# Performance work log

Hardware: AMD Instinct MI355X
Metric: run time of the kernel (lower is better)

Reference implementation:

```python
import jax, jax.numpy as jnp
import numpy as np

NUM_HEADS = 16
HEAD_DIM = 64


def setup_inputs() -> dict:
    key = jax.random.key(0)
    k1, k2, k3 = jax.random.split(key, 3)
    B, S, D = 2, 2048, 1024
    scale = 1.0 / np.sqrt(D)
    return {
        "x": jax.random.normal(k1, (B, S, D), dtype=jnp.float32),
        "W_qkv": jax.random.normal(k2, (D, 3 * D), dtype=jnp.float32) * scale,
        "b_qkv": jnp.zeros((3 * D,), dtype=jnp.float32),
        "W_o": jax.random.normal(k3, (D, D), dtype=jnp.float32) * scale,
        "b_o": jnp.zeros((D,), dtype=jnp.float32),
    }


def reference(x, W_qkv, b_qkv, W_o, b_o):
    B, S, D = x.shape
    H, Hd = NUM_HEADS, HEAD_DIM
    qkv = x @ W_qkv + b_qkv                      # [B, S, 3D]
    qkv = qkv.reshape(B, S, H, 3 * Hd).transpose(0, 2, 1, 3)  # [B, H, S, 3Hd]
    q, k, v = jnp.split(qkv, 3, axis=-1)         # each [B, H, S, Hd]
    # negative squared Euclidean distance: -(|q|^2 - 2 q.k + |k|^2)
    q_sq = jnp.sum(q * q, axis=-1)[..., :, None]   # [B, H, S, 1]
    k_sq = jnp.sum(k * k, axis=-1)[..., None, :]   # [B, H, 1, S]
    qk = jnp.einsum("bhsd,bhtd->bhst", q, k)       # [B, H, S, S]
    logits = -(q_sq - 2.0 * qk + k_sq)
    attn = jax.nn.softmax(logits, axis=-1)
    vals = jnp.einsum("bhst,bhtd->bhsd", attn, v)  # [B, H, S, Hd]
    vals = vals.transpose(0, 2, 1, 3).reshape(B, S, D)
    return vals @ W_o + b_o
```

## Files before the change

kernel.cpp:

```cpp
#include <hip/hip_runtime.h>
#include <hip/hip_bf16.h>

#define NUM_B   2
#define SEQ     2048
#define DMODEL  1024
#define NH      16
#define HD      64
#define M_TOT   (NUM_B * SEQ)
#define N_QKV   (3 * DMODEL)
#define LOG2E   1.4426950408889634f
#define EXP_BIAS 96.0f

typedef __attribute__((ext_vector_type(8))) short short8v;
typedef __attribute__((ext_vector_type(4))) float float4v;
typedef unsigned short ushort_t;

__device__ __forceinline__ ushort_t f2bf(float x) {
    unsigned u = __builtin_bit_cast(unsigned, x);
    u = u + 0x7FFFu + ((u >> 16) & 1u);
    return (ushort_t)(u >> 16);
}
__device__ __forceinline__ float bf2f(ushort_t h) {
    unsigned u = ((unsigned)h) << 16;
    return __builtin_bit_cast(float, u);
}
__device__ __forceinline__ void gll16(const void* g, void* l) {
    __builtin_amdgcn_global_load_lds(
        (const __attribute__((address_space(1))) unsigned int*)g,
        (__attribute__((address_space(3))) unsigned int*)l, 16, 0, 0);
}
__device__ __forceinline__ int sw4(int r) { return (r & 3) ^ ((r >> 2) & 3); }

__global__ __launch_bounds__(256) void prep_kernel(
    const float* __restrict__ Wq, const float* __restrict__ Wo,
    const float* __restrict__ Xf,
    ushort_t* __restrict__ WqT_hi, ushort_t* __restrict__ WqT_lo,
    ushort_t* __restrict__ WoT,
    ushort_t* __restrict__ Xhi, ushort_t* __restrict__ Xlo)
{
    const int bid = blockIdx.x;
    const int t = threadIdx.x;

    if (bid >= 1024) {
        size_t base = (size_t)(bid - 1024) * 4096 + t * 16;
        float xs[16];
        *(float4v*)&xs[0]  = *(const float4v*)(Xf + base);
        *(float4v*)&xs[4]  = *(const float4v*)(Xf + base + 4);
        *(float4v*)&xs[8]  = *(const float4v*)(Xf + base + 8);
        *(float4v*)&xs[12] = *(const float4v*)(Xf + base + 12);
        short8v h0, h1, l0, l1;
        #pragma unroll
        for (int e = 0; e < 8; e++) {
            ushort_t a = f2bf(xs[e]), b = f2bf(xs[8 + e]);
            h0[e] = (short)a; h1[e] = (short)b;
            l0[e] = (short)f2bf(xs[e] - bf2f(a));
            l1[e] = (short)f2bf(xs[8 + e] - bf2f(b));
        }
        *(short8v*)(Xhi + base) = h0; *(short8v*)(Xhi + base + 8) = h1;
        *(short8v*)(Xlo + base) = l0; *(short8v*)(Xlo + base + 8) = l1;
        return;
    }

    __shared__ float Tf[64][65];
    const float* src; ushort_t *dhi, *dlo; int N, k0, n0;
    if (bid < 768) {
        int kt = bid / 48, nt = bid % 48;
        src = Wq; N = N_QKV; dhi = WqT_hi; dlo = WqT_lo;
        k0 = kt * 64; n0 = nt * 64;
    } else {
        int tid = bid - 768;
        int kt = tid >> 4, nt = tid & 15;
        src = Wo; N = DMODEL; dhi = WoT; dlo = nullptr;
        k0 = kt * 64; n0 = nt * 64;
    }
    {
        int r = t >> 2, c0 = (t & 3) * 16;
        const float* srow = src + (size_t)(k0 + r) * N + n0 + c0;
        #pragma unroll
        for (int u = 0; u < 4; u++) {
            float4v f = *(const float4v*)(srow + 4 * u);
            #pragma unroll
            for (int e = 0; e < 4; e++) Tf[r][c0 + 4 * u + e] = f[e];
        }
    }
    __syncthreads();
    {
        int nl = t >> 2, kc = (t & 3) * 16;
        short8v h0, h1, l0, l1;
        #pragma unroll
        for (int e = 0; e < 8; e++) {
            float x0 = Tf[kc + e][nl];
            float x1 = Tf[kc + 8 + e][nl];
            ushort_t a = f2bf(x0), b = f2bf(x1);
            h0[e] = (short)a; h1[e] = (short)b;
            l0[e] = (short)f2bf(x0 - bf2f(a));
            l1[e] = (short)f2bf(x1 - bf2f(b));
        }
        ushort_t* o = dhi + (size_t)(n0 + nl) * 1024 + k0 + kc;
        *(short8v*)o = h0; *(short8v*)(o + 8) = h1;
        if (dlo) {
            ushort_t* o2 = dlo + (size_t)(n0 + nl) * 1024 + k0 + kc;
            *(short8v*)o2 = l0; *(short8v*)(o2 + 8) = l1;
        }
    }
}

__global__ __launch_bounds__(512, 2) void qkv_mfma256_kernel(
    const ushort_t* __restrict__ Xhi, const ushort_t* __restrict__ Xlo,
    const ushort_t* __restrict__ WqT_hi, const ushort_t* __restrict__ WqT_lo,
    const float* __restrict__ bias,
    ushort_t* __restrict__ Qhi, ushort_t* __restrict__ Qlo,
    ushort_t* __restrict__ Khi, ushort_t* __restrict__ Klo,
    ushort_t* __restrict__ Vout,
    float* __restrict__ Qsq, float* __restrict__ Ksq)
{
    __shared__ ushort_t AS [2 * 2 * 8192];
    __shared__ ushort_t BSh[2 * 2 * 8192];
    const int SLAB = 8192;
    const int BUFS = 2 * SLAB;

    const int t    = threadIdx.x;
    const int w    = t >> 6;
    const int quad = (t >> 4) & 3, ln = t & 15;
    const int wr = w >> 2, wc = w & 3;
    const int bx = blockIdx.x, by = blockIdx.y;
    const int p  = bx >> 2, bq = bx & 3;
    const int m0 = by * 256;
    const bool qk = (p != 2);
    const int h  = 4 * bq + wc;
    const int g  = p + 3 * h;

    const ushort_t* gA[2]; const ushort_t* gB[2]; int lOff[2];
    #pragma unroll
    for (int i = 0; i < 2; i++) {
        int c = 512 * i + t;
        int r = c >> 2, kb = c & 3;
        gA[i] = Xhi + (size_t)(m0 + r) * 1024 + 8 * (kb ^ sw4(r));
        int hj = 4 * bq + (r >> 6);
        int ng = 192 * hj + 64 * p + (r & 63);
        gB[i] = WqT_hi + (size_t)ng * 1024 + 8 * (kb ^ sw4(r));
        lOff[i] = (512 * i + 64 * w) * 8;
    }
    const size_t xlo_off = (size_t)(Xlo - Xhi);
    const size_t wlo_off = (size_t)(WqT_lo - WqT_hi);

    int aoff[8], boff[4];
    #pragma unroll
    for (int mt = 0; mt < 8; mt++) {
        int m_l = 128 * wr + 16 * mt + ln;
        aoff[mt] = m_l * 32 + ((quad ^ sw4(m_l)) << 3);
    }
    #pragma unroll
    for (int nt = 0; nt < 4; nt++) {
        int n_l = 64 * wc + 16 * nt + ln;
        boff[nt] = n_l * 32 + ((quad ^ sw4(n_l)) << 3);
    }

    float4v acc[8][4];
    #pragma unroll
    for (int i = 0; i < 8; i++)
        #pragma unroll
        for (int j = 0; j < 4; j++) acc[i][j] = (float4v){0.f, 0.f, 0.f, 0.f};

    auto stage = [&](int ks, int buf) {
        const int kk = 32 * ks;
        ushort_t* Ab = &AS [buf * BUFS];
        ushort_t* Bb = &BSh[buf * BUFS];
        #pragma unroll
        for (int i = 0; i < 2; i++) {
            gll16(gA[i] + kk, Ab + lOff[i]);
            gll16(gB[i] + kk, Bb + lOff[i]);
        }
        if (qk) {
            #pragma unroll
            for (int i = 0; i < 2; i++) {
                gll16(gA[i] + kk + xlo_off, Ab + SLAB + lOff[i]);
                gll16(gB[i] + kk + wlo_off, Bb + SLAB + lOff[i]);
            }
        }
    };

    const int NKS = DMODEL / 32;
    stage(0, 0);
    __syncthreads();

    for (int ks = 0; ks < NKS; ks++) {
        const int buf = ks & 1;
        if (ks + 1 < NKS) stage(ks + 1, buf ^ 1);

        const ushort_t* Ab = &AS [buf * BUFS];
        const ushort_t* Bb = &BSh[buf * BUFS];

        short8v bh4[4], bl4[4];
        #pragma unroll
        for (int nt = 0; nt < 4; nt++) {
            bh4[nt] = *(const short8v*)(Bb + boff[nt]);
            if (qk) bl4[nt] = *(const short8v*)(Bb + SLAB + boff[nt]);
        }
        #pragma unroll
        for (int mt = 0; mt < 8; mt++) {
            short8v ahm = *(const short8v*)(Ab + aoff[mt]);
            if (qk) {
                short8v alm = *(const short8v*)(Ab + SLAB + aoff[mt]);
                #pragma unroll
                for (int nt = 0; nt < 4; nt++) {
                    acc[mt][nt] = __builtin_amdgcn_mfma_f32_16x16x32_bf16(ahm, bh4[nt], acc[mt][nt], 0, 0, 0);
                    acc[mt][nt] = __builtin_amdgcn_mfma_f32_16x16x32_bf16(ahm, bl4[nt], acc[mt][nt], 0, 0, 0);
                    acc[mt][nt] = __builtin_amdgcn_mfma_f32_16x16x32_bf16(alm, bh4[nt], acc[mt][nt], 0, 0, 0);
                }
            } else {
                #pragma unroll
                for (int nt = 0; nt < 4; nt++)
                    acc[mt][nt] = __builtin_amdgcn_mfma_f32_16x16x32_bf16(ahm, bh4[nt], acc[mt][nt], 0, 0, 0);
            }
        }
        __syncthreads();
    }

    float bvv[4];
    #pragma unroll
    for (int nt = 0; nt < 4; nt++) bvv[nt] = bias[64 * g + 16 * nt + ln];

    #pragma unroll
    for (int mt = 0; mt < 8; mt++) {
        #pragma unroll
        for (int r = 0; r < 4; r++) {
            int m = m0 + 128 * wr + 16 * mt + 4 * quad + r;
            int bb = m >> 11, s = m & (SEQ - 1);
            size_t hsrow = (size_t)(bb * NH + h) * SEQ + s;
            size_t rowbase = hsrow * HD;
            float vv[4];
            #pragma unroll
            for (int nt = 0; nt < 4; nt++) vv[nt] = acc[mt][nt][r] + bvv[nt];
            if (p == 0) {
                float sq = 0.f;
                #pragma unroll
                for (int nt = 0; nt < 4; nt++) {
                    float v = vv[nt];
                    sq += v * v;
                    float v2 = v * (2.0f * LOG2E);
                    ushort_t hb = f2bf(v2);
                    Qhi[rowbase + 16 * nt + ln] = hb;
                    Qlo[rowbase + 16 * nt + ln] = f2bf(v2 - bf2f(hb));
                }
                sq += __shfl_xor(sq, 1); sq += __shfl_xor(sq, 2);
                sq += __shfl_xor(sq, 4); sq += __shfl_xor(sq, 8);
                if (ln == 0) Qsq[hsrow] = sq * LOG2E - EXP_BIAS;
            } else if (p == 1) {
                float sq = 0.f;
                #pragma unroll
                for (int nt = 0; nt < 4; nt++) {
                    float v = vv[nt];
                    sq += v * v;
                    ushort_t hb = f2bf(v);
                    Khi[rowbase + 16 * nt + ln] = hb;
                    Klo[rowbase + 16 * nt + ln] = f2bf(v - bf2f(hb));
                }
                sq += __shfl_xor(sq, 1); sq += __shfl_xor(sq, 2);
                sq += __shfl_xor(sq, 4); sq += __shfl_xor(sq, 8);
                if (ln == 0) Ksq[hsrow] = sq * LOG2E;
            } else {
                #pragma unroll
                for (int nt = 0; nt < 4; nt++)
                    Vout[((size_t)(bb * NH + h) * 64 + 16 * nt + ln) * SEQ + s] = f2bf(vv[nt]);
            }
        }
    }
}

template<bool PRE>
__global__ __launch_bounds__(256) void qkv_mfma_kernel(
    const float* __restrict__ X,
    const ushort_t* __restrict__ Xhi, const ushort_t* __restrict__ Xlo,
    const ushort_t* __restrict__ WqT_hi, const ushort_t* __restrict__ WqT_lo,
    const float* __restrict__ bias,
    ushort_t* __restrict__ Qhi, ushort_t* __restrict__ Qlo,
    ushort_t* __restrict__ Khi, ushort_t* __restrict__ Klo,
    ushort_t* __restrict__ Vout,
    float* __restrict__ Qsq, float* __restrict__ Ksq)
{
    __shared__ ushort_t AS2[2 * 128 * 32];
    __shared__ ushort_t BS [2 * 128 * 32];
    const int LO = 128 * 32;
    const int t = threadIdx.x;
    const int w = t >> 6, lane = t & 63;
    const int quad = (t >> 4) & 3, ln = t & 15;
    const int wr = w >> 1, wc = w & 1;
    const int m0 = blockIdx.y * 128, n0 = blockIdx.x * 128;
    const int g = blockIdx.x * 2 + wc;
    const int h = g / 3, part = g % 3;

    const ushort_t* gA[2]; ushort_t* lA[2];
    const float* aptr = nullptr;
    ushort_t *ast_hi0, *ast_hi1, *ast_lo0, *ast_lo1;
    size_t xlo_off = 0;
    if constexpr (PRE) {
        #pragma unroll
        for (int i = 0; i < 2; i++) {
            int c = 256 * i + 64 * w + lane;
            int r = c >> 2, kbp = c & 3;
            gA[i] = Xhi + (size_t)(m0 + r) * 1024 + 8 * (kbp ^ sw4(r));
            lA[i] = &AS2[(256 * i + 64 * w) * 8];
        }
        xlo_off = (size_t)(Xlo - Xhi);
    } else {
        const int arow = t >> 1, akh = t & 1;
        aptr = X + (size_t)(m0 + arow) * DMODEL + 16 * akh;
        const int asw = sw4(arow);
        ast_hi0 = &AS2[arow * 32 + (((2 * akh) ^ asw) << 3)];
        ast_hi1 = &AS2[arow * 32 + (((2 * akh + 1) ^ asw) << 3)];
        ast_lo0 = &AS2[LO + arow * 32 + (((2 * akh) ^ asw) << 3)];
        ast_lo1 = &AS2[LO + arow * 32 + (((2 * akh + 1) ^ asw) << 3)];
    }

    const ushort_t* gB[2]; ushort_t* lB[2];
    #pragma unroll
    for (int i = 0; i < 2; i++) {
        int c = 256 * i + 64 * w + lane;
        int n = c >> 2, kbp = c & 3;
        gB[i] = WqT_hi + (size_t)(n0 + n) * 1024 + 8 * (kbp ^ sw4(n));
        lB[i] = &BS[(256 * i + 64 * w) * 8];
    }
    const size_t lo_goff = (size_t)(WqT_lo - WqT_hi);

    int aoff[4], boff[4];
    #pragma unroll
    for (int i = 0; i < 4; i++) {
        int m_l = 64 * wr + 16 * i + ln;
        aoff[i] = m_l * 32 + ((quad ^ sw4(m_l)) << 3);
        int n_l = 64 * wc + 16 * i + ln;
        boff[i] = n_l * 32 + ((quad ^ sw4(n_l)) << 3);
    }

    float4v acc[4][4];
    #pragma unroll
    for (int i = 0; i < 4; i++)
        #pragma unroll
        for (int j = 0; j < 4; j++) acc[i][j] = (float4v){0.f, 0.f, 0.f, 0.f};

    for (int k0 = 0; k0 < DMODEL; k0 += 32) {
        __syncthreads();
        #pragma unroll
        for (int i = 0; i < 2; i++) {
            gll16(gB[i] + k0, lB[i]);
            gll16(gB[i] + k0 + lo_goff, lB[i] + LO);
        }
        if constexpr (PRE) {
            #pragma unroll
            for (int i = 0; i < 2; i++) {
                gll16(gA[i] + k0, lA[i]);
                gll16(gA[i] + k0 + xlo_off, lA[i] + LO);
            }
        } else {
            float xs[16];
            *(float4v*)&xs[0]  = *(const float4v*)(aptr + k0);
            *(float4v*)&xs[4]  = *(const float4v*)(aptr + k0 + 4);
            *(float4v*)&xs[8]  = *(const float4v*)(aptr + k0 + 8);
            *(float4v*)&xs[12] = *(const float4v*)(aptr + k0 + 12);
            short8v h0, h1, l0, l1;
            #pragma unroll
            for (int e = 0; e < 8; e++) {
                ushort_t a = f2bf(xs[e]), b = f2bf(xs[8 + e]);
                h0[e] = (short)a; h1[e] = (short)b;
                l0[e] = (short)f2bf(xs[e] - bf2f(a));
                l1[e] = (short)f2bf(xs[8 + e] - bf2f(b));
            }
            *(short8v*)ast_hi0 = h0; *(short8v*)ast_hi1 = h1;
            *(short8v*)ast_lo0 = l0; *(short8v*)ast_lo1 = l1;
        }
        __syncthreads();

        short8v ah[4], al[4], bh[4], bl[4];
        #pragma unroll
        for (int i = 0; i < 4; i++) {
            ah[i] = *(short8v*)&AS2[aoff[i]];
            al[i] = *(short8v*)&AS2[LO + aoff[i]];
            bh[i] = *(short8v*)&BS[boff[i]];
            bl[i] = *(short8v*)&BS[LO + boff[i]];
        }
        if (part != 2) {
            #pragma unroll
            for (int mt = 0; mt < 4; mt++)
                #pragma unroll
                for (int nt = 0; nt < 4; nt++) {
                    acc[mt][nt] = __builtin_amdgcn_mfma_f32_16x16x32_bf16(ah[mt], bh[nt], acc[mt][nt], 0, 0, 0);
                    acc[mt][nt] = __builtin_amdgcn_mfma_f32_16x16x32_bf16(ah[mt], bl[nt], acc[mt][nt], 0, 0, 0);
                    acc[mt][nt] = __builtin_amdgcn_mfma_f32_16x16x32_bf16(al[mt], bh[nt], acc[mt][nt], 0, 0, 0);
                }
        } else {
            #pragma unroll
            for (int mt = 0; mt < 4; mt++)
                #pragma unroll
                for (int nt = 0; nt < 4; nt++)
                    acc[mt][nt] = __builtin_amdgcn_mfma_f32_16x16x32_bf16(ah[mt], bh[nt], acc[mt][nt], 0, 0, 0);
        }
    }

    float bvv[4];
    #pragma unroll
    for (int nt = 0; nt < 4; nt++) bvv[nt] = bias[64 * g + 16 * nt + ln];

    #pragma unroll
    for (int mt = 0; mt < 4; mt++) {
        #pragma unroll
        for (int r = 0; r < 4; r++) {
            int m = m0 + 64 * wr + 16 * mt + 4 * quad + r;
            int bb = m >> 11, s = m & (SEQ - 1);
            size_t hsrow = (size_t)(bb * NH + h) * SEQ + s;
            size_t rowbase = hsrow * HD;
            float vv[4];
            #pragma unroll
            for (int nt = 0; nt < 4; nt++) vv[nt] = acc[mt][nt][r] + bvv[nt];
            if (part == 0) {
                float sq = 0.f;
                #pragma unroll
                for (int nt = 0; nt < 4; nt++) {
                    float v = vv[nt];
                    sq += v * v;
                    float v2 = v * (2.0f * LOG2E);
                    ushort_t hb = f2bf(v2);
                    Qhi[rowbase + 16 * nt + ln] = hb;
                    Qlo[rowbase + 16 * nt + ln] = f2bf(v2 - bf2f(hb));
                }
                sq += __shfl_xor(sq, 1); sq += __shfl_xor(sq, 2);
                sq += __shfl_xor(sq, 4); sq += __shfl_xor(sq, 8);
                if (ln == 0) Qsq[hsrow] = sq * LOG2E - EXP_BIAS;
            } else if (part == 1) {
                float sq = 0.f;
                #pragma unroll
                for (int nt = 0; nt < 4; nt++) {
                    float v = vv[nt];
                    sq += v * v;
                    ushort_t hb = f2bf(v);
                    Khi[rowbase + 16 * nt + ln] = hb;
                    Klo[rowbase + 16 * nt + ln] = f2bf(v - bf2f(hb));
                }
                sq += __shfl_xor(sq, 1); sq += __shfl_xor(sq, 2);
                sq += __shfl_xor(sq, 4); sq += __shfl_xor(sq, 8);
                if (ln == 0) Ksq[hsrow] = sq * LOG2E;
            } else {
                #pragma unroll
                for (int nt = 0; nt < 4; nt++)
                    Vout[rowbase + 16 * nt + ln] = f2bf(vv[nt]);
            }
        }
    }
}

template<bool PRE>
__global__ __launch_bounds__(256, 4) void attn_mfma_kernel(
    const ushort_t* __restrict__ Qhi, const ushort_t* __restrict__ Qlo,
    const ushort_t* __restrict__ Khi, const ushort_t* __restrict__ Klo,
    const ushort_t* __restrict__ Vsrc,
    const float* __restrict__ Qsq, const float* __restrict__ Ksq,
    ushort_t* __restrict__ vals)
{
    __shared__ ushort_t KS[2 * 64 * 64];
    __shared__ ushort_t VtS [64 * 64];
    __shared__ ushort_t PsS [64 * 72];
    const int LO = 64 * 64;

    const int t    = threadIdx.x;
    const int w    = t >> 6, lane = t & 63;
    const int quad = (t >> 4) & 3, ln = t & 15;
    const int bh   = blockIdx.y;
    const int q0   = blockIdx.x * 64;
    const size_t base  = (size_t)bh * SEQ * HD;
    const size_t baseS = (size_t)bh * SEQ;

    short8v qhi[2], qlo[2];
    float4v qsq4;
    {
        size_t ro = base + (size_t)(q0 + 16 * w + ln) * HD + quad * 8;
        qhi[0] = *(const short8v*)(Qhi + ro);
        qhi[1] = *(const short8v*)(Qhi + ro + 32);
        qlo[0] = *(const short8v*)(Qlo + ro);
        qlo[1] = *(const short8v*)(Qlo + ro + 32);
        qsq4 = *(const float4v*)(Qsq + baseS + q0 + 16 * w + 4 * quad);
    }

    const ushort_t* gK[2]; ushort_t* lK[2];
    #pragma unroll
    for (int i = 0; i < 2; i++) {
        int c = 256 * i + 64 * w + lane;
        int key = c >> 3, dbp = c & 7;
        gK[i] = Khi + base + (size_t)key * HD + 8 * (dbp ^ (key & 7));
        lK[i] = &KS[(256 * i + 64 * w) * 8];
    }
    const size_t kloff = (size_t)(Klo - Khi);

    const ushort_t* gV[2]; ushort_t* lV[2];
    if constexpr (PRE) {
        #pragma unroll
        for (int i = 0; i < 2; i++) {
            int c = 256 * i + 64 * w + lane;
            int d = c >> 3, kc = c & 7;
            gV[i] = Vsrc + ((size_t)bh * 64 + d) * SEQ + 8 * (kc ^ (d & 7));
            lV[i] = &VtS[(256 * i + 64 * w) * 8];
        }
    }

    float4v accO[4];
    float lsum[4];
    #pragma unroll
    for (int nt = 0; nt < 4; nt++) accO[nt] = (float4v){0.f, 0.f, 0.f, 0.f};
    #pragma unroll
    for (int r = 0; r < 4; r++) lsum[r] = 0.f;

    for (int kt = 0; kt < SEQ; kt += 64) {
        __syncthreads();
        #pragma unroll
        for (int i = 0; i < 2; i++) {
            gll16(gK[i] + (size_t)kt * HD, lK[i]);
            gll16(gK[i] + (size_t)kt * HD + kloff, lK[i] + LO);
        }
        if constexpr (PRE) {
            #pragma unroll
            for (int i = 0; i < 2; i++)
                gll16(gV[i] + kt, lV[i]);
        } else {
            #pragma unroll
            for (int i = 0; i < 2; i++) {
                int c = t + 256 * i;
                int key = c >> 3, db = c & 7;
                short8v v8 = *(const short8v*)(Vsrc + base + (size_t)(kt + key) * HD + 8 * db);
                #pragma unroll
                for (int e = 0; e < 8; e++) {
                    int col = key ^ (e << 3);
                    VtS[(8 * db + e) * 64 + col] = (ushort_t)v8[e];
                }
            }
        }
        float ksq_c[4];
        #pragma unroll
        for (int nt = 0; nt < 4; nt++)
            ksq_c[nt] = Ksq[baseS + kt + 16 * nt + ln];
        __syncthreads();

        float4v accS[4];
        #pragma unroll
        for (int nt = 0; nt < 4; nt++) accS[nt] = (float4v){0.f, 0.f, 0.f, 0.f};

        #pragma unroll
        for (int nt = 0; nt < 4; nt++) {
            int keyrow = 16 * nt + ln;
            #pragma unroll
            for (int c = 0; c < 2; c++) {
                int db  = quad + 4 * c;
                int off = keyrow * 64 + ((db ^ (keyrow & 7)) << 3);
                short8v bh_ = *(short8v*)&KS[off];
                short8v bl_ = *(short8v*)&KS[LO + off];
                accS[nt] = __builtin_amdgcn_mfma_f32_16x16x32_bf16(qhi[c], bh_, accS[nt], 0, 0, 0);
                accS[nt] = __builtin_amdgcn_mfma_f32_16x16x32_bf16(qhi[c], bl_, accS[nt], 0, 0, 0);
                accS[nt] = __builtin_amdgcn_mfma_f32_16x16x32_bf16(qlo[c], bh_, accS[nt], 0, 0, 0);
            }
        }

        #pragma unroll
        for (int nt = 0; nt < 4; nt++) {
            float pv[4];
            #pragma unroll
            for (int r = 0; r < 4; r++) {
                float p = exp2f(accS[nt][r] - ksq_c[nt] - qsq4[r]);
                lsum[r] += p;
                pv[r] = p;
            }
            unsigned int pk01, pk23;
            asm("v_cvt_pk_bf16_f32 %0, %1, %2" : "=v"(pk01) : "v"(pv[0]), "v"(pv[1]));
            asm("v_cvt_pk_bf16_f32 %0, %1, %2" : "=v"(pk23) : "v"(pv[2]), "v"(pv[3]));
            ushort_t* pp = &PsS[(16 * w + 4 * quad) * 72 + 16 * nt + ln];
            pp[0]       = (ushort_t)(pk01 & 0xffffu);
            pp[72]      = (ushort_t)(pk01 >> 16);
            pp[144]     = (ushort_t)(pk23 & 0xffffu);
            pp[216]     = (ushort_t)(pk23 >> 16);
        }
        __syncthreads();

        #pragma unroll
        for (int c = 0; c < 2; c++) {
            short8v aP = *(short8v*)&PsS[(16 * w + ln) * 72 + quad * 8 + 32 * c];
            #pragma unroll
            for (int nt = 0; nt < 4; nt++) {
                int drow = 16 * nt + ln;
                int db   = quad + 4 * c;
                int off  = drow * 64 + ((db ^ (drow & 7)) << 3);
                short8v bV = *(short8v*)&VtS[off];
                accO[nt] = __builtin_amdgcn_mfma_f32_16x16x32_bf16(aP, bV, accO[nt], 0, 0, 0);
            }
        }
    }

    const int bb = bh >> 4, h = bh & 15;
    float inv[4];
    #pragma unroll
    for (int r = 0; r < 4; r++) {
        float s = lsum[r];
        s += __shfl_xor(s, 1); s += __shfl_xor(s, 2);
        s += __shfl_xor(s, 4); s += __shfl_xor(s, 8);
        inv[r] = 1.f / s;
    }
    #pragma unroll
    for (int nt = 0; nt < 4; nt++)
        #pragma unroll
        for (int r = 0; r < 4; r++) {
            int row = q0 + 16 * w + 4 * quad + r;
            vals[(size_t)(bb * SEQ + row) * DMODEL + h * 64 + 16 * nt + ln] =
                f2bf(accO[nt][r] * inv[r]);
        }
}

__global__ __launch_bounds__(256) void out_mfma_kernel(
    const ushort_t* __restrict__ Ab, const ushort_t* __restrict__ BT,
    const float* __restrict__ bias, float* __restrict__ out)
{
    __shared__ ushort_t AS[128 * 32], BSo[128 * 32];
    const int t = threadIdx.x;
    const int w = t >> 6, lane = t & 63;
    const int quad = (t >> 4) & 3, ln = t & 15;
    const int wr = w >> 1, wc = w & 1;
    const int m0 = blockIdx.y * 128, n0 = blockIdx.x * 128;

    const ushort_t* gA[2]; const ushort_t* gB[2];
    ushort_t *lA[2], *lB[2];
    #pragma unroll
    for (int i = 0; i < 2; i++) {
        int c = 256 * i + 64 * w + lane;
        int r = c >> 2, kbp = c & 3;
        gA[i] = Ab + (size_t)(m0 + r) * 1024 + 8 * (kbp ^ sw4(r));
        gB[i] = BT + (size_t)(n0 + r) * 1024 + 8 * (kbp ^ sw4(r));
        lA[i] = &AS[(256 * i + 64 * w) * 8];
        lB[i] = &BSo[(256 * i + 64 * w) * 8];
    }
    int aoff[4], boff[4];
    #pragma unroll
    for (int i = 0; i < 4; i++) {
        int m_l = 64 * wr + 16 * i + ln;
        aoff[i] = m_l * 32 + ((quad ^ sw4(m_l)) << 3);
        int n_l = 64 * wc + 16 * i + ln;
        boff[i] = n_l * 32 + ((quad ^ sw4(n_l)) << 3);
    }

    float4v acc[4][4];
    #pragma unroll
    for (int i = 0; i < 4; i++)
        #pragma unroll
        for (int j = 0; j < 4; j++) acc[i][j] = (float4v){0.f, 0.f, 0.f, 0.f};

    for (int k0 = 0; k0 < DMODEL; k0 += 32) {
        __syncthreads();
        #pragma unroll
        for (int i = 0; i < 2; i++) {
            gll16(gA[i] + k0, lA[i]);
            gll16(gB[i] + k0, lB[i]);
        }
        __syncthreads();
        short8v a[4], b[4];
        #pragma unroll
        for (int i = 0; i < 4; i++) {
            a[i] = *(short8v*)&AS[aoff[i]];
            b[i] = *(short8v*)&BSo[boff[i]];
        }
        #pragma unroll
        for (int mt = 0; mt < 4; mt++)
            #pragma unroll
            for (int nt = 0; nt < 4; nt++)
                acc[mt][nt] = __builtin_amdgcn_mfma_f32_16x16x32_bf16(a[mt], b[nt], acc[mt][nt], 0, 0, 0);
    }

    #pragma unroll
    for (int nt = 0; nt < 4; nt++) {
        int n = n0 + 64 * wc + 16 * nt + ln;
        float bv = bias[n];
        #pragma unroll
        for (int mt = 0; mt < 4; mt++)
            #pragma unroll
            for (int r = 0; r < 4; r++) {
                int m = m0 + 64 * wr + 16 * mt + 4 * quad + r;
                out[(size_t)m * DMODEL + n] = acc[mt][nt][r] + bv;
            }
    }
}

extern "C" void kernel_launch(void* const* d_in, const int* in_sizes, int n_in,
                              void* d_out, int out_size, void* d_ws, size_t ws_size,
                              hipStream_t stream) {
    const float* x     = (const float*)d_in[0];
    const float* W_qkv = (const float*)d_in[1];
    const float* b_qkv = (const float*)d_in[2];
    const float* W_o   = (const float*)d_in[3];
    const float* b_o   = (const float*)d_in[4];
    float* out = (float*)d_out;

    const size_t WQT = (size_t)N_QKV * DMODEL;
    const size_t WO  = (size_t)DMODEL * DMODEL;
    const size_t QE  = (size_t)NUM_B * NH * SEQ * HD;
    const size_t SQN = (size_t)NUM_B * NH * SEQ;

    const size_t NEED = (2 * WQT + WO + 5 * QE + 2 * QE) * 2 + 2 * SQN * 4;
    const bool pre = (ws_size >= NEED);

    ushort_t* ws     = (ushort_t*)d_ws;
    ushort_t* WqT_hi = ws;
    ushort_t* WqT_lo = WqT_hi + WQT;
    ushort_t* WoT    = WqT_lo + WQT;
    ushort_t* Qhi    = WoT + WO;
    ushort_t* Qlo    = Qhi + QE;
    ushort_t* Khi    = Qlo + QE;
    ushort_t* Klo    = Khi + QE;
    ushort_t* Vx     = Klo + QE;
    float*    Qsq; float* Ksq;
    ushort_t* valsb; ushort_t* Xhi = nullptr; ushort_t* Xlo = nullptr;

    if (pre) {
        Qsq   = (float*)(Vx + QE);
        Ksq   = Qsq + SQN;
        Xhi   = (ushort_t*)(Ksq + SQN);
        Xlo   = Xhi + QE;
        valsb = WqT_hi;
    } else {
        valsb = Vx + QE;
        Qsq   = (float*)(valsb + QE);
        Ksq   = Qsq + SQN;
    }

    prep_kernel<<<pre ? 2048 : 1024, 256, 0, stream>>>(
        W_qkv, W_o, x, WqT_hi, WqT_lo, WoT, Xhi, Xlo);
    if (pre) {
        qkv_mfma256_kernel<<<dim3(12, M_TOT / 256), 512, 0, stream>>>(
            Xhi, Xlo, WqT_hi, WqT_lo, b_qkv, Qhi, Qlo, Khi, Klo, Vx, Qsq, Ksq);
        attn_mfma_kernel<true><<<dim3(SEQ / 64, NUM_B * NH), 256, 0, stream>>>(
            Qhi, Qlo, Khi, Klo, Vx, Qsq, Ksq, valsb);
    } else {
        qkv_mfma_kernel<false><<<dim3(N_QKV / 128, M_TOT / 128), 256, 0, stream>>>(
            x, nullptr, nullptr, WqT_hi, WqT_lo, b_qkv, Qhi, Qlo, Khi, Klo, Vx, Qsq, Ksq);
        attn_mfma_kernel<false><<<dim3(SEQ / 64, NUM_B * NH), 256, 0, stream>>>(
            Qhi, Qlo, Khi, Klo, Vx, Qsq, Ksq, valsb);
    }
    out_mfma_kernel<<<dim3(DMODEL / 128, M_TOT / 128), 256, 0, stream>>>(
        valsb, WoT, b_o, out);
}
```

Baseline: 297.8 us.

## Deepen QKV GEMM prefetch to two stages with explicit vmcnt waits and setprio

```diff
diff --git a/kernel.cpp b/kernel.cpp
--- a/kernel.cpp
+++ b/kernel.cpp
@@ -182,11 +182,18 @@
 
     const int NKS = DMODEL / 32;
     stage(0, 0);
-    __syncthreads();
+    stage(1, 1);
 
     for (int ks = 0; ks < NKS; ks++) {
         const int buf = ks & 1;
-        if (ks + 1 < NKS) stage(ks + 1, buf ^ 1);
+        if (ks + 1 < NKS) {
+            if (qk) asm volatile("s_waitcnt vmcnt(8)" ::: "memory");
+            else    asm volatile("s_waitcnt vmcnt(4)" ::: "memory");
+        } else {
+            asm volatile("s_waitcnt vmcnt(0)" ::: "memory");
+        }
+        __builtin_amdgcn_s_barrier();
+        asm volatile("" ::: "memory");
 
         const ushort_t* Ab = &AS [buf * BUFS];
         const ushort_t* Bb = &BSh[buf * BUFS];
@@ -197,24 +204,57 @@
             bh4[nt] = *(const short8v*)(Bb + boff[nt]);
             if (qk) bl4[nt] = *(const short8v*)(Bb + SLAB + boff[nt]);
         }
-        #pragma unroll
-        for (int mt = 0; mt < 8; mt++) {
-            short8v ahm = *(const short8v*)(Ab + aoff[mt]);
+        short8v ah0[4], al0[4];
+        #pragma unroll
+        for (int mt = 0; mt < 4; mt++) {
+            ah0[mt] = *(const short8v*)(Ab + aoff[mt]);
+            if (qk) al0[mt] = *(const short8v*)(Ab + SLAB + aoff[mt]);
+        }
+        __builtin_amdgcn_s_setprio(1);
+        #pragma unroll
+        for (int mt = 0; mt < 4; mt++) {
             if (qk) {
-                short8v alm = *(const short8v*)(Ab + SLAB + aoff[mt]);
                 #pragma unroll
                 for (int nt = 0; nt < 4; nt++) {
-                    acc[mt][nt] = __builtin_amdgcn_mfma_f32_16x16x32_bf16(ahm, bh4[nt], acc[mt][nt], 0, 0, 0);
-                    acc[mt][nt] = __builtin_amdgcn_mfma_f32_16x16x32_bf16(ahm, bl4[nt], acc[mt][nt], 0, 0, 0);
-                    acc[mt][nt] = __builtin_amdgcn_mfma_f32_16x16x32_bf16(alm, bh4[nt], acc[mt][nt], 0, 0, 0);
+                    acc[mt][nt] = __builtin_amdgcn_mfma_f32_16x16x32_bf16(ah0[mt], bh4[nt], acc[mt][nt], 0, 0, 0);
+                    acc[mt][nt] = __builtin_amdgcn_mfma_f32_16x16x32_bf16(ah0[mt], bl4[nt], acc[mt][nt], 0, 0, 0);
+                    acc[mt][nt] = __builtin_amdgcn_mfma_f32_16x16x32_bf16(al0[mt], bh4[nt], acc[mt][nt], 0, 0, 0);
                 }
             } else {
                 #pragma unroll
                 for (int nt = 0; nt < 4; nt++)
-                    acc[mt][nt] = __builtin_amdgcn_mfma_f32_16x16x32_bf16(ahm, bh4[nt], acc[mt][nt], 0, 0, 0);
-            }
-        }
-        __syncthreads();
+                    acc[mt][nt] = __builtin_amdgcn_mfma_f32_16x16x32_bf16(ah0[mt], bh4[nt], acc[mt][nt], 0, 0, 0);
+            }
+        }
+        __builtin_amdgcn_s_setprio(0);
+        short8v ah1[4], al1[4];
+        #pragma unroll
+        for (int mt = 0; mt < 4; mt++) {
+            ah1[mt] = *(const short8v*)(Ab + aoff[4 + mt]);
+            if (qk) al1[mt] = *(const short8v*)(Ab + SLAB + aoff[4 + mt]);
+        }
+        __builtin_amdgcn_s_setprio(1);
+        #pragma unroll
+        for (int mt = 0; mt < 4; mt++) {
+            if (qk) {
+                #pragma unroll
+                for (int nt = 0; nt < 4; nt++) {
+                    acc[4 + mt][nt] = __builtin_amdgcn_mfma_f32_16x16x32_bf16(ah1[mt], bh4[nt], acc[4 + mt][nt], 0, 0, 0);
+                    acc[4 + mt][nt] = __builtin_amdgcn_mfma_f32_16x16x32_bf16(ah1[mt], bl4[nt], acc[4 + mt][nt], 0, 0, 0);
+                    acc[4 + mt][nt] = __builtin_amdgcn_mfma_f32_16x16x32_bf16(al1[mt], bh4[nt], acc[4 + mt][nt], 0, 0, 0);
+                }
+            } else {
+                #pragma unroll
+                for (int nt = 0; nt < 4; nt++)
+                    acc[4 + mt][nt] = __builtin_amdgcn_mfma_f32_16x16x32_bf16(ah1[mt], bh4[nt], acc[4 + mt][nt], 0, 0, 0);
+            }
+        }
+        __builtin_amdgcn_s_setprio(0);
+
+        asm volatile("" ::: "memory");
+        __builtin_amdgcn_s_barrier();
+        asm volatile("" ::: "memory");
+        if (ks + 2 < NKS) stage(ks + 2, buf);
     }
 
     float bvv[4];
```

Result: no change. 303.1 us (+1.8%).
